# Performance work log

Hardware: AMD Instinct MI355X
Metric: run time of the kernel (lower is better)

The kernel has to match this reference:

```python
import jax, jax.numpy as jnp
import numpy as np

DIM = 768      # model dim
H = 12         # heads
HD = DIM // H  # head dim = 64
T = 8          # num_frames // 2 (video temporal frames)
SF = 8         # spec_frames (audio temporal frames)
AP = 196       # audio patches per frame
VP = 196       # video patches per frame
B = 4          # batch
SCALE = HD ** (-0.5)  # 0.125


def setup_inputs() -> dict:
    key = jax.random.key(0)
    ks = jax.random.split(key, 12)
    n = lambda k, shape, s=1.0: s * jax.random.normal(k, shape, dtype=jnp.float32)
    return {
        "s_x": n(ks[0], (2 + AP, B * SF, DIM)),
        "t_x": n(ks[1], (1 + VP, B * T, DIM)),
        "clip_space_pos": n(ks[2], (AP, DIM), SCALE),
        "vmae_space_pos": n(ks[3], (VP, DIM), SCALE),
        "clip_temporal_pos": n(ks[4], (SF, DIM), SCALE),
        "vmae_temporal_pos": n(ks[5], (T, DIM), SCALE),
        "q_w": n(ks[6], (DIM, DIM), 0.02),
        "q_b": jnp.zeros((DIM,), jnp.float32),
        "kv_w": n(ks[7], (2 * DIM, DIM), 0.02),
        "kv_b": jnp.zeros((2 * DIM,), jnp.float32),
        "proj_w": n(ks[8], (DIM, DIM), 0.02),
        "proj_b": jnp.zeros((DIM,), jnp.float32),
    }


def _prep(pat, space_pos, temp_pos, tt):
    # pat: (n, b*tt, d) ; rearrange 'n (b t) d -> b t n d', add space pos,
    # 'b t n d -> b n t d', add temporal pos, 'b n t d -> b (n t) d'
    n, bt, d = pat.shape
    b = bt // tt
    x = pat.reshape(n, b, tt, d).transpose(1, 2, 0, 3)      # b t n d
    x = x + space_pos                                        # (n,d) bcast
    x = x.transpose(0, 2, 1, 3) + temp_pos                   # b n t d + (t,d)
    return x.reshape(b, n * tt, d)


def reference(s_x, t_x, clip_space_pos, vmae_space_pos, clip_temporal_pos,
              vmae_temporal_pos, q_w, q_b, kv_w, kv_b, proj_w, proj_b):
    t_x_cls = t_x[:1]                                        # (1, b*T, d)
    s_pat = _prep(s_x[2:], clip_space_pos, clip_temporal_pos, SF)   # (b, AP*SF, d)
    t_pat = _prep(t_x[1:], vmae_space_pos, vmae_temporal_pos, T)    # (b, VP*T, d)

    b, N, d = t_pat.shape
    M = s_pat.shape[1]
    q = t_pat @ q_w.T + q_b                                  # (b, N, d)
    q = q.reshape(b, N, H, HD).transpose(0, 2, 1, 3)         # b h n hd
    kv = s_pat @ kv_w.T + kv_b                               # (b, M, 2d)
    kv = kv.reshape(b, M, 2, H, HD).transpose(2, 0, 3, 1, 4) # 2 b h m hd
    k, v = kv[0], kv[1]

    attn = jax.nn.softmax(jnp.einsum('bhnd,bhmd->bhnm', q * SCALE, k), axis=-1)
    out = jnp.einsum('bhnm,bhmd->bhnd', attn, v)             # b h n hd
    out = out.transpose(0, 2, 1, 3).reshape(b, N, d)         # b n d
    out = out @ proj_w.T + proj_b

    # 'b (n t) d -> n (b t) d'
    out = out.reshape(b, VP, T, d).transpose(1, 0, 2, 3).reshape(VP, b * T, d)
    return jnp.concatenate([t_x_cls, out], axis=0)           # (1+VP, b*T, d)
```

## Files before the change

### kernel.cpp

```cpp
#include <hip/hip_runtime.h>
#include <hip/hip_bf16.h>

#define DIM 768
#define NH 12
#define HD 64
#define NSEQ 1568
#define ROWS 6272
#define QSC2 0.18033688011112042f
#define AST 72

typedef __attribute__((ext_vector_type(8))) short short8;
typedef __attribute__((ext_vector_type(4))) float f32x4;
typedef __attribute__((ext_vector_type(4))) unsigned short u16x4;
typedef unsigned short ushort_t;
typedef unsigned int uint_t;

static __device__ __forceinline__ ushort_t f2bf(float f) {
    union { float f; uint_t u; } c; c.f = f;
    uint_t u = c.u + 0x7fffu + ((c.u >> 16) & 1u);
    return (ushort_t)(u >> 16);
}
static __device__ __forceinline__ int cvt_pk_bf16(float lo, float hi) {
    int r;
    asm("v_cvt_pk_bf16_f32 %0, %1, %2" : "=v"(r) : "v"(lo), "v"(hi));
    return r;
}
static __device__ __forceinline__ void glds16(const short* g, short* l) {
    __builtin_amdgcn_global_load_lds(
        (const __attribute__((address_space(1))) void*)g,
        (__attribute__((address_space(3))) void*)l, 16, 0, 0);
}

#define SM_HALF(S, PF, LR)                                                    \
    {                                                                         \
        float p_[4][4];                                                       \
        _Pragma("unroll")                                                     \
        for (int jb = 0; jb < 4; ++jb) {                                      \
            _Pragma("unroll")                                                 \
            for (int r = 0; r < 4; ++r)                                       \
                p_[jb][r] = __builtin_amdgcn_exp2f(S[jb][r]);                 \
        }                                                                     \
        float rs_ = ((p_[0][0] + p_[0][1]) + (p_[0][2] + p_[0][3]))           \
                  + ((p_[1][0] + p_[1][1]) + (p_[1][2] + p_[1][3]))           \
                  + ((p_[2][0] + p_[2][1]) + (p_[2][2] + p_[2][3]))           \
                  + ((p_[3][0] + p_[3][1]) + (p_[3][2] + p_[3][3]));          \
        rs_ += __shfl_xor(rs_, 16);                                           \
        rs_ += __shfl_xor(rs_, 32);                                           \
        LR += rs_;                                                            \
        int pw_[4][2];                                                        \
        _Pragma("unroll")                                                     \
        for (int jb = 0; jb < 4; ++jb) {                                      \
            pw_[jb][0] = cvt_pk_bf16(p_[jb][0], p_[jb][1]);                   \
            pw_[jb][1] = cvt_pk_bf16(p_[jb][2], p_[jb][3]);                   \
        }                                                                     \
        _Pragma("unroll")                                                     \
        for (int jb2 = 0; jb2 < 2; ++jb2) {                                   \
            int S0_ = gh ? pw_[jb2 * 2 + 1][0] : pw_[jb2 * 2][0];             \
            int S1_ = gh ? pw_[jb2 * 2 + 1][1] : pw_[jb2 * 2][1];             \
            union { int i[4]; short8 s; } fr_;                                \
            fr_.i[0] = __builtin_amdgcn_ds_bpermute(addr0, S0_);              \
            fr_.i[1] = __builtin_amdgcn_ds_bpermute(addr0, S1_);              \
            fr_.i[2] = __builtin_amdgcn_ds_bpermute(addr1, S0_);              \
            fr_.i[3] = __builtin_amdgcn_ds_bpermute(addr1, S1_);              \
            PF[jb2] = fr_.s;                                                  \
        }                                                                     \
    }

#define PREP_HALF (ROWS * (DIM / 8))
__global__ __launch_bounds__(256)
void prep2_bf(const float* __restrict__ src_t, const float* __restrict__ src_s,
              const float* __restrict__ vsp, const float* __restrict__ csp,
              const float* __restrict__ vtp, const float* __restrict__ ctp,
              short* __restrict__ dst_t, short* __restrict__ dst_s) {
    int idx = blockIdx.x * 256 + threadIdx.x;
    if (idx >= 2 * PREP_HALF) return;
    int sel = idx >= PREP_HALF;
    int i0  = sel ? idx - PREP_HALF : idx;
    const float* src  = sel ? src_s : src_t;
    const float* spos = sel ? csp : vsp;
    const float* tpos = sel ? ctp : vtp;
    short* dst = sel ? dst_s : dst_t;
    int d8  = i0 % (DIM / 8);
    int row = i0 / (DIM / 8);
    int b = row / NSEQ;
    int i = row % NSEQ;
    int n = i >> 3;
    int t = i & 7;
    const float4* s4 = reinterpret_cast<const float4*>(src + ((size_t)n * 32 + b * 8 + t) * DIM + d8 * 8);
    const float4* p4 = reinterpret_cast<const float4*>(spos + (size_t)n * DIM + d8 * 8);
    const float4* q4 = reinterpret_cast<const float4*>(tpos + (size_t)t * DIM + d8 * 8);
    union { int w[4]; short8 v; } o;
    float4 a0 = s4[0], a1 = s4[1], b0 = p4[0], b1 = p4[1], c0 = q4[0], c1 = q4[1];
    o.w[0] = cvt_pk_bf16(a0.x + b0.x + c0.x, a0.y + b0.y + c0.y);
    o.w[1] = cvt_pk_bf16(a0.z + b0.z + c0.z, a0.w + b0.w + c0.w);
    o.w[2] = cvt_pk_bf16(a1.x + b1.x + c1.x, a1.y + b1.y + c1.y);
    o.w[3] = cvt_pk_bf16(a1.z + b1.z + c1.z, a1.w + b1.w + c1.w);
    reinterpret_cast<short8*>(dst)[i0] = o.v;
}

#define W8 (DIM * DIM / 8)
__global__ __launch_bounds__(256)
void conv3_bf(const float* __restrict__ qw, const float* __restrict__ kvw,
              const float* __restrict__ pw, short* __restrict__ dq,
              short* __restrict__ dkv, short* __restrict__ dp) {
    int idx = blockIdx.x * 256 + threadIdx.x;
    if (idx >= 4 * W8) return;
    const float* src; short* dst; int off;
    if (idx < W8)            { src = qw;  dst = dq;  off = idx; }
    else if (idx < 3 * W8)   { src = kvw; dst = dkv; off = idx - W8; }
    else                     { src = pw;  dst = dp;  off = idx - 3 * W8; }
    const float4* s4 = reinterpret_cast<const float4*>(src + (size_t)off * 8);
    float4 a0 = s4[0], a1 = s4[1];
    union { int w[4]; short8 v; } o;
    o.w[0] = cvt_pk_bf16(a0.x, a0.y);
    o.w[1] = cvt_pk_bf16(a0.z, a0.w);
    o.w[2] = cvt_pk_bf16(a1.x, a1.y);
    o.w[3] = cvt_pk_bf16(a1.z, a1.w);
    reinterpret_cast<short8*>(dst)[off] = o.v;
}

__global__ __launch_bounds__(256)
void cls_kernel(const float* __restrict__ src, float* __restrict__ dst) {
    int idx = blockIdx.x * 256 + threadIdx.x;
    if (idx < 32 * DIM / 4)
        reinterpret_cast<float4*>(dst)[idx] = reinterpret_cast<const float4*>(src)[idx];
}

__global__ __launch_bounds__(256)
void gemm_qkv(const short* __restrict__ tpat, const short* __restrict__ spat,
              const short* __restrict__ wq, const short* __restrict__ wkv,
              const float* __restrict__ q_b, const float* __restrict__ kv_b,
              ushort_t* __restrict__ qout, ushort_t* __restrict__ kout,
              ushort_t* __restrict__ vtout) {
    __shared__ short As[128 * 32];
    __shared__ short Ws[128 * 32];
    const int t = threadIdx.x;
    const int l = t & 63, w = t >> 6;
    const int li = l & 15, g = l >> 4;
    const int mode = (blockIdx.x >= 6);
    const short* A  = mode ? spat : tpat;
    const short* Wm = mode ? wkv : wq;
    const float* bias = mode ? kv_b : q_b;
    const int c0 = (mode ? (int)blockIdx.x - 6 : (int)blockIdx.x) * 128;
    const int r0 = blockIdx.y * 128;
    const int wrow = (w >> 1) * 64, wcol = (w & 1) * 64;

    f32x4 acc[4][4];
    #pragma unroll
    for (int i = 0; i < 4; ++i)
        #pragma unroll
        for (int j = 0; j < 4; ++j) acc[i][j] = (f32x4){0.f, 0.f, 0.f, 0.f};

    const short* Ag = A  + (size_t)(r0 + w * 32 + (l >> 2)) * DIM + (l & 3) * 8;
    const short* Wg = Wm + (size_t)(c0 + w * 32 + (l >> 2)) * DIM + (l & 3) * 8;
    short* Al0 = &As[(w * 32) * 32];
    short* Al1 = &As[(w * 32 + 16) * 32];
    short* Wl0 = &Ws[(w * 32) * 32];
    short* Wl1 = &Ws[(w * 32 + 16) * 32];

    for (int k0 = 0; k0 < DIM; k0 += 32) {
        glds16(Ag + k0,                       Al0);
        glds16(Ag + (size_t)16 * DIM + k0,    Al1);
        glds16(Wg + k0,                       Wl0);
        glds16(Wg + (size_t)16 * DIM + k0,    Wl1);
        __syncthreads();
        short8 af[4], wf[4];
        #pragma unroll
        for (int mi = 0; mi < 4; ++mi)
            af[mi] = *reinterpret_cast<const short8*>(&As[(wrow + mi * 16 + li) * 32 + g * 8]);
        #pragma unroll
        for (int ni = 0; ni < 4; ++ni)
            wf[ni] = *reinterpret_cast<const short8*>(&Ws[(wcol + ni * 16 + li) * 32 + g * 8]);
        __builtin_amdgcn_s_setprio(1);
        #pragma unroll
        for (int mi = 0; mi < 4; ++mi)
            #pragma unroll
            for (int ni = 0; ni < 4; ++ni)
                acc[mi][ni] = __builtin_amdgcn_mfma_f32_16x16x32_bf16(af[mi], wf[ni], acc[mi][ni], 0, 0, 0);
        __builtin_amdgcn_s_setprio(0);
        __syncthreads();
    }

    #pragma unroll
    for (int mi = 0; mi < 4; ++mi) {
        int rowbase = r0 + wrow + mi * 16 + g * 4;
        int b = rowbase / NSEQ;
        int ii = rowbase - b * NSEQ;
        #pragma unroll
        for (int ni = 0; ni < 4; ++ni) {
            int c = c0 + wcol + ni * 16 + li;
            float bv = bias[c];
            if (mode == 0) {
                int h = c >> 6, e = c & 63;
                size_t base = (((size_t)b * NH + h) * NSEQ + ii) * HD + e;
                #pragma unroll
                for (int rr = 0; rr < 4; ++rr)
                    qout[base + (size_t)rr * HD] = f2bf((acc[mi][ni][rr] + bv) * QSC2);
            } else {
                if (c < DIM) {
                    int h = c >> 6, e = c & 63;
                    size_t base = (((size_t)b * NH + h) * NSEQ + ii) * HD + e;
                    #pragma unroll
                    for (int rr = 0; rr < 4; ++rr)
                        kout[base + (size_t)rr * HD] = f2bf(acc[mi][ni][rr] + bv);
                } else {
                    int cc = c - DIM;
                    int h = cc >> 6, e = cc & 63;
                    union { int w2[2]; u16x4 v; } pk;
                    pk.w2[0] = cvt_pk_bf16(acc[mi][ni][0] + bv, acc[mi][ni][1] + bv);
                    pk.w2[1] = cvt_pk_bf16(acc[mi][ni][2] + bv, acc[mi][ni][3] + bv);
                    *reinterpret_cast<u16x4*>(vtout + (((size_t)b * NH + h) * HD + e) * NSEQ + ii) = pk.v;
                }
            }
        }
    }
}

__global__ __launch_bounds__(256)
void gemm_proj(const short* __restrict__ A, const short* __restrict__ Wm,
               const float* __restrict__ bias, float* __restrict__ out) {
    __shared__ short As[128 * 32];
    __shared__ short Ws[128 * 32];
    const int t = threadIdx.x;
    const int l = t & 63, w = t >> 6;
    const int li = l & 15, g = l >> 4;
    const int c0 = blockIdx.x * 128, r0 = blockIdx.y * 128;
    const int wrow = (w >> 1) * 64, wcol = (w & 1) * 64;

    f32x4 acc[4][4];
    #pragma unroll
    for (int i = 0; i < 4; ++i)
        #pragma unroll
        for (int j = 0; j < 4; ++j) acc[i][j] = (f32x4){0.f, 0.f, 0.f, 0.f};

    const short* Ag = A  + (size_t)(r0 + w * 32 + (l >> 2)) * DIM + (l & 3) * 8;
    const short* Wg = Wm + (size_t)(c0 + w * 32 + (l >> 2)) * DIM + (l & 3) * 8;
    short* Al0 = &As[(w * 32) * 32];
    short* Al1 = &As[(w * 32 + 16) * 32];
    short* Wl0 = &Ws[(w * 32) * 32];
    short* Wl1 = &Ws[(w * 32 + 16) * 32];

    for (int k0 = 0; k0 < DIM; k0 += 32) {
        glds16(Ag + k0,                       Al0);
        glds16(Ag + (size_t)16 * DIM + k0,    Al1);
        glds16(Wg + k0,                       Wl0);
        glds16(Wg + (size_t)16 * DIM + k0,    Wl1);
        __syncthreads();
        short8 af[4], wf[4];
        #pragma unroll
        for (int mi = 0; mi < 4; ++mi)
            af[mi] = *reinterpret_cast<const short8*>(&As[(wrow + mi * 16 + li) * 32 + g * 8]);
        #pragma unroll
        for (int ni = 0; ni < 4; ++ni)
            wf[ni] = *reinterpret_cast<const short8*>(&Ws[(wcol + ni * 16 + li) * 32 + g * 8]);
        __builtin_amdgcn_s_setprio(1);
        #pragma unroll
        for (int mi = 0; mi < 4; ++mi)
            #pragma unroll
            for (int ni = 0; ni < 4; ++ni)
                acc[mi][ni] = __builtin_amdgcn_mfma_f32_16x16x32_bf16(af[mi], wf[ni], acc[mi][ni], 0, 0, 0);
        __builtin_amdgcn_s_setprio(0);
        __syncthreads();
    }

    #pragma unroll
    for (int mi = 0; mi < 4; ++mi) {
        int rowbase = r0 + wrow + mi * 16 + g * 4;
        int b = rowbase / NSEQ;
        int ii = rowbase - b * NSEQ;
        #pragma unroll
        for (int ni = 0; ni < 4; ++ni) {
            int c = c0 + wcol + ni * 16 + li;
            float bv = bias[c];
            #pragma unroll
            for (int rr = 0; rr < 4; ++rr) {
                int i2 = ii + rr;
                int n = i2 >> 3, tt = i2 & 7;
                out[((size_t)(1 + n) * 32 + b * 8 + tt) * DIM + c] = acc[mi][ni][rr] + bv;
            }
        }
    }
}

__global__ __launch_bounds__(256)
void attn_bf(const short* __restrict__ q, const short* __restrict__ k,
             const short* __restrict__ vt, ushort_t* __restrict__ ao) {
    __shared__ short Ks[2 * 64 * AST];
    __shared__ short Vs[2 * 64 * AST];
    const int t = threadIdx.x, l = t & 63, w = t >> 6;
    const int li = l & 15, g = l >> 4;
    const int bh = blockIdx.y, b = bh / NH, h = bh % NH;
    const int q0 = blockIdx.x * 128;
    const short* qb = q + (size_t)bh * NSEQ * HD;
    const short* kb = k + (size_t)bh * NSEQ * HD;
    const short* vb = vt + (size_t)bh * HD * NSEQ;
    const int row = t >> 2, ch = t & 3;

    short8 qf0[2], qf1[2];
    {
        int r_ = q0 + w * 32 + li;
        int rs = (r_ < NSEQ) ? r_ : 0;
        const short* s = qb + (size_t)rs * HD + g * 8;
        qf0[0] = *reinterpret_cast<const short8*>(s);
        qf0[1] = *reinterpret_cast<const short8*>(s + 32);
        r_ += 16;
        rs = (r_ < NSEQ) ? r_ : 0;
        s = qb + (size_t)rs * HD + g * 8;
        qf1[0] = *reinterpret_cast<const short8*>(s);
        qf1[1] = *reinterpret_cast<const short8*>(s + 32);
    }

    short8 kr0, kr1, vr0, vr1;
    {
        const short* s = kb + (size_t)row * HD + ch * 16;
        kr0 = *reinterpret_cast<const short8*>(s);
        kr1 = *reinterpret_cast<const short8*>(s + 8);
        const short* vs = vb + (size_t)row * NSEQ + ch * 16;
        vr0 = *reinterpret_cast<const short8*>(vs);
        vr1 = *reinterpret_cast<const short8*>(vs + 8);
    }
    *reinterpret_cast<short8*>(&Ks[row * AST + ch * 16])     = kr0;
    *reinterpret_cast<short8*>(&Ks[row * AST + ch * 16 + 8]) = kr1;
    *reinterpret_cast<short8*>(&Vs[row * AST + ch * 16])     = vr0;
    *reinterpret_cast<short8*>(&Vs[row * AST + ch * 16 + 8]) = vr1;

    f32x4 o0[4], o1[4];
    #pragma unroll
    for (int i = 0; i < 4; ++i) {
        o0[i] = (f32x4){0.f, 0.f, 0.f, 0.f};
        o1[i] = (f32x4){0.f, 0.f, 0.f, 0.f};
    }
    float lr0 = 0.f, lr1 = 0.f;
    const int addr0 = (li + ((2 * g) & 3) * 16) * 4;
    const int addr1 = (li + ((2 * g + 1) & 3) * 16) * 4;
    const int gh = g >> 1;

    int cur = 0;
    for (int m0 = 0; m0 < NSEQ; m0 += 64, cur ^= 1) {
        const short* Kc = &Ks[cur * 64 * AST];
        const short* Vc = &Vs[cur * 64 * AST];
        short* Kn = &Ks[(cur ^ 1) * 64 * AST];
        short* Vn = &Vs[(cur ^ 1) * 64 * AST];
        __syncthreads();
        const int m1 = m0 + 64;
        if (m1 < NSEQ) {
            int rs = (m1 + row < NSEQ) ? m1 + row : 0;
            const short* s = kb + (size_t)rs * HD + ch * 16;
            kr0 = *reinterpret_cast<const short8*>(s);
            kr1 = *reinterpret_cast<const short8*>(s + 8);
            int cs = (m1 + ch * 16 < NSEQ) ? ch : 0;
            const short* vs = vb + (size_t)row * NSEQ + m1 + cs * 16;
            vr0 = *reinterpret_cast<const short8*>(vs);
            vr1 = *reinterpret_cast<const short8*>(vs + 8);
        }

        f32x4 s0[4], s1[4];
        #pragma unroll
        for (int i = 0; i < 4; ++i) {
            s0[i] = (f32x4){0.f, 0.f, 0.f, 0.f};
            s1[i] = (f32x4){0.f, 0.f, 0.f, 0.f};
        }
        __builtin_amdgcn_s_setprio(1);
        #pragma unroll
        for (int jb = 0; jb < 4; ++jb) {
            short8 kf0 = *reinterpret_cast<const short8*>(&Kc[(jb * 16 + li) * AST + g * 8]);
            short8 kf1 = *reinterpret_cast<const short8*>(&Kc[(jb * 16 + li) * AST + 32 + g * 8]);
            s0[jb] = __builtin_amdgcn_mfma_f32_16x16x32_bf16(kf0, qf0[0], s0[jb], 0, 0, 0);
            s0[jb] = __builtin_amdgcn_mfma_f32_16x16x32_bf16(kf1, qf0[1], s0[jb], 0, 0, 0);
            s1[jb] = __builtin_amdgcn_mfma_f32_16x16x32_bf16(kf0, qf1[0], s1[jb], 0, 0, 0);
            s1[jb] = __builtin_amdgcn_mfma_f32_16x16x32_bf16(kf1, qf1[1], s1[jb], 0, 0, 0);
        }
        __builtin_amdgcn_s_setprio(0);
        if (m0 + 64 > NSEQ) {
            #pragma unroll
            for (int jb = 0; jb < 4; ++jb)
                #pragma unroll
                for (int r = 0; r < 4; ++r)
                    if (m0 + jb * 16 + g * 4 + r >= NSEQ) {
                        s0[jb][r] = -1e30f;
                        s1[jb][r] = -1e30f;
                    }
        }

        short8 pf0[2], pf1[2];
        SM_HALF(s0, pf0, lr0)
        SM_HALF(s1, pf1, lr1)

        if (m1 < NSEQ) {
            *reinterpret_cast<short8*>(&Kn[row * AST + ch * 16])     = kr0;
            *reinterpret_cast<short8*>(&Kn[row * AST + ch * 16 + 8]) = kr1;
            *reinterpret_cast<short8*>(&Vn[row * AST + ch * 16])     = vr0;
            *reinterpret_cast<short8*>(&Vn[row * AST + ch * 16 + 8]) = vr1;
        }

        __builtin_amdgcn_s_setprio(1);
        #pragma unroll
        for (int nb = 0; nb < 4; ++nb)
            #pragma unroll
            for (int jb2 = 0; jb2 < 2; ++jb2) {
                short8 vf = *reinterpret_cast<const short8*>(&Vc[(nb * 16 + li) * AST + jb2 * 32 + g * 8]);
                o0[nb] = __builtin_amdgcn_mfma_f32_16x16x32_bf16(vf, pf0[jb2], o0[nb], 0, 0, 0);
                o1[nb] = __builtin_amdgcn_mfma_f32_16x16x32_bf16(vf, pf1[jb2], o1[nb], 0, 0, 0);
            }
        __builtin_amdgcn_s_setprio(0);
    }

    {
        int orow = q0 + w * 32 + li;
        if (orow < NSEQ) {
            float invl = 1.f / lr0;
            ushort_t* ob = ao + ((size_t)b * NSEQ + orow) * DIM + h * HD;
            #pragma unroll
            for (int nb = 0; nb < 4; ++nb) {
                union { int w2[2]; u16x4 v; } pk;
                pk.w2[0] = cvt_pk_bf16(o0[nb][0] * invl, o0[nb][1] * invl);
                pk.w2[1] = cvt_pk_bf16(o0[nb][2] * invl, o0[nb][3] * invl);
                *reinterpret_cast<u16x4*>(ob + nb * 16 + g * 4) = pk.v;
            }
        }
    }
    {
        int orow = q0 + w * 32 + 16 + li;
        if (orow < NSEQ) {
            float invl = 1.f / lr1;
            ushort_t* ob = ao + ((size_t)b * NSEQ + orow) * DIM + h * HD;
            #pragma unroll
            for (int nb = 0; nb < 4; ++nb) {
                union { int w2[2]; u16x4 v; } pk;
                pk.w2[0] = cvt_pk_bf16(o1[nb][0] * invl, o1[nb][1] * invl);
                pk.w2[1] = cvt_pk_bf16(o1[nb][2] * invl, o1[nb][3] * invl);
                *reinterpret_cast<u16x4*>(ob + nb * 16 + g * 4) = pk.v;
            }
        }
    }
}

extern "C" void kernel_launch(void* const* d_in, const int* in_sizes, int n_in,
                              void* d_out, int out_size, void* d_ws, size_t ws_size,
                              hipStream_t stream) {
    const float* s_x    = (const float*)d_in[0];
    const float* t_x    = (const float*)d_in[1];
    const float* csp    = (const float*)d_in[2];
    const float* vsp    = (const float*)d_in[3];
    const float* ctp    = (const float*)d_in[4];
    const float* vtp    = (const float*)d_in[5];
    const float* q_w    = (const float*)d_in[6];
    const float* q_b    = (const float*)d_in[7];
    const float* kv_w   = (const float*)d_in[8];
    const float* kv_b   = (const float*)d_in[9];
    const float* proj_w = (const float*)d_in[10];
    const float* proj_b = (const float*)d_in[11];
    float* out = (float*)d_out;

    const size_t S2 = (size_t)ROWS * DIM;
    short* tpat = (short*)d_ws;
    short* spat = tpat + S2;
    short* qbf  = spat + S2;
    short* kbf  = qbf + S2;
    short* vtbf = kbf + S2;
    short* wq   = vtbf + S2;
    short* wkv  = wq + (size_t)DIM * DIM;
    short* wp   = wkv + (size_t)2 * DIM * DIM;

    prep2_bf<<<(2 * PREP_HALF + 255) / 256, 256, 0, stream>>>(
        t_x + (size_t)32 * DIM, s_x + (size_t)64 * DIM, vsp, csp, vtp, ctp, tpat, spat);
    conv3_bf<<<(4 * W8 + 255) / 256, 256, 0, stream>>>(q_w, kv_w, proj_w, wq, wkv, wp);
    cls_kernel<<<24, 256, 0, stream>>>(t_x, out);

    gemm_qkv<<<dim3(18, 49), 256, 0, stream>>>(tpat, spat, wq, wkv, q_b, kv_b,
                                               (ushort_t*)qbf, (ushort_t*)kbf, (ushort_t*)vtbf);
    attn_bf<<<dim3(13, 48), 256, 0, stream>>>(qbf, kbf, vtbf, (ushort_t*)tpat);
    gemm_proj<<<dim3(6, 49), 256, 0, stream>>>(tpat, wp, proj_b, out);
}
```

Measured before the change: 152.0 us.

## Split attention KV range in two and merge partial outputs in a new kernel

The attention kernel now splits the key/value sequence into two ranges via a third grid dimension. Each half writes unnormalized fp32 partial outputs and row sums to workspace. A new merge kernel adds the two halves, normalizes and writes bf16 output. This doubles the number of blocks to improve CU occupancy and wave balance, at the cost of extra fp32 global traffic and one more kernel launch.

```diff
diff --git a/kernel.cpp b/kernel.cpp
--- a/kernel.cpp
+++ b/kernel.cpp
@@ -8,6 +8,7 @@
 #define ROWS 6272
 #define QSC2 0.18033688011112042f
 #define AST 72
+#define SPLIT_M 832
 
 typedef __attribute__((ext_vector_type(8))) short short8;
 typedef __attribute__((ext_vector_type(4))) float f32x4;
@@ -284,12 +285,16 @@
 
 __global__ __launch_bounds__(256)
 void attn_bf(const short* __restrict__ q, const short* __restrict__ k,
-             const short* __restrict__ vt, ushort_t* __restrict__ ao) {
+             const short* __restrict__ vt, float* __restrict__ opart,
+             float* __restrict__ lpart) {
     __shared__ short Ks[2 * 64 * AST];
     __shared__ short Vs[2 * 64 * AST];
     const int t = threadIdx.x, l = t & 63, w = t >> 6;
     const int li = l & 15, g = l >> 4;
-    const int bh = blockIdx.y, b = bh / NH, h = bh % NH;
+    const int bh = blockIdx.y;
+    const int sp = blockIdx.z;
+    const int m_start = sp ? SPLIT_M : 0;
+    const int m_end   = sp ? NSEQ : SPLIT_M;
     const int q0 = blockIdx.x * 128;
     const short* qb = q + (size_t)bh * NSEQ * HD;
     const short* kb = k + (size_t)bh * NSEQ * HD;
@@ -312,10 +317,10 @@
 
     short8 kr0, kr1, vr0, vr1;
     {
-        const short* s = kb + (size_t)row * HD + ch * 16;
+        const short* s = kb + (size_t)(m_start + row) * HD + ch * 16;
         kr0 = *reinterpret_cast<const short8*>(s);
         kr1 = *reinterpret_cast<const short8*>(s + 8);
-        const short* vs = vb + (size_t)row * NSEQ + ch * 16;
+        const short* vs = vb + (size_t)row * NSEQ + m_start + ch * 16;
         vr0 = *reinterpret_cast<const short8*>(vs);
         vr1 = *reinterpret_cast<const short8*>(vs + 8);
     }
@@ -336,14 +341,14 @@
     const int gh = g >> 1;
 
     int cur = 0;
-    for (int m0 = 0; m0 < NSEQ; m0 += 64, cur ^= 1) {
+    for (int m0 = m_start; m0 < m_end; m0 += 64, cur ^= 1) {
         const short* Kc = &Ks[cur * 64 * AST];
         const short* Vc = &Vs[cur * 64 * AST];
         short* Kn = &Ks[(cur ^ 1) * 64 * AST];
         short* Vn = &Vs[(cur ^ 1) * 64 * AST];
         __syncthreads();
         const int m1 = m0 + 64;
-        if (m1 < NSEQ) {
+        if (m1 < m_end) {
             int rs = (m1 + row < NSEQ) ? m1 + row : 0;
             const short* s = kb + (size_t)rs * HD + ch * 16;
             kr0 = *reinterpret_cast<const short8*>(s);
@@ -386,7 +391,7 @@
         SM_HALF(s0, pf0, lr0)
         SM_HALF(s1, pf1, lr1)
 
-        if (m1 < NSEQ) {
+        if (m1 < m_end) {
             *reinterpret_cast<short8*>(&Kn[row * AST + ch * 16])     = kr0;
             *reinterpret_cast<short8*>(&Kn[row * AST + ch * 16 + 8]) = kr1;
             *reinterpret_cast<short8*>(&Vn[row * AST + ch * 16])     = vr0;
@@ -408,31 +413,48 @@
     {
         int orow = q0 + w * 32 + li;
         if (orow < NSEQ) {
-            float invl = 1.f / lr0;
-            ushort_t* ob = ao + ((size_t)b * NSEQ + orow) * DIM + h * HD;
-            #pragma unroll
-            for (int nb = 0; nb < 4; ++nb) {
-                union { int w2[2]; u16x4 v; } pk;
-                pk.w2[0] = cvt_pk_bf16(o0[nb][0] * invl, o0[nb][1] * invl);
-                pk.w2[1] = cvt_pk_bf16(o0[nb][2] * invl, o0[nb][3] * invl);
-                *reinterpret_cast<u16x4*>(ob + nb * 16 + g * 4) = pk.v;
-            }
+            float* op = opart + (((size_t)sp * 48 + bh) * NSEQ + orow) * HD + g * 4;
+            #pragma unroll
+            for (int nb = 0; nb < 4; ++nb)
+                *reinterpret_cast<f32x4*>(op + nb * 16) = o0[nb];
         }
     }
     {
         int orow = q0 + w * 32 + 16 + li;
         if (orow < NSEQ) {
-            float invl = 1.f / lr1;
-            ushort_t* ob = ao + ((size_t)b * NSEQ + orow) * DIM + h * HD;
-            #pragma unroll
-            for (int nb = 0; nb < 4; ++nb) {
-                union { int w2[2]; u16x4 v; } pk;
-                pk.w2[0] = cvt_pk_bf16(o1[nb][0] * invl, o1[nb][1] * invl);
-                pk.w2[1] = cvt_pk_bf16(o1[nb][2] * invl, o1[nb][3] * invl);
-                *reinterpret_cast<u16x4*>(ob + nb * 16 + g * 4) = pk.v;
-            }
-        }
-    }
+            float* op = opart + (((size_t)sp * 48 + bh) * NSEQ + orow) * HD + g * 4;
+            #pragma unroll
+            for (int nb = 0; nb < 4; ++nb)
+                *reinterpret_cast<f32x4*>(op + nb * 16) = o1[nb];
+        }
+    }
+    if (l < 16) {
+        int r_ = q0 + w * 32 + l;
+        float* lp = lpart + ((size_t)sp * 48 + bh) * NSEQ;
+        if (r_ < NSEQ)      lp[r_]      = lr0;
+        if (r_ + 16 < NSEQ) lp[r_ + 16] = lr1;
+    }
+}
+
+__global__ __launch_bounds__(256)
+void merge_bf(const float* __restrict__ opart, const float* __restrict__ lpart,
+              ushort_t* __restrict__ ao) {
+    const int bh = blockIdx.y;
+    int tid = blockIdx.x * 256 + threadIdx.x;
+    int row = tid >> 4, e4 = (tid & 15) * 4;
+    const size_t base = ((size_t)bh * NSEQ + row) * HD + e4;
+    const size_t so = (size_t)48 * NSEQ * HD;
+    f32x4 a = *reinterpret_cast<const f32x4*>(opart + base);
+    f32x4 c = *reinterpret_cast<const f32x4*>(opart + so + base);
+    float l0 = lpart[(size_t)bh * NSEQ + row];
+    float l1 = lpart[(size_t)48 * NSEQ + (size_t)bh * NSEQ + row];
+    float inv = 1.f / (l0 + l1);
+    int b = bh / NH, h = bh - b * NH;
+    ushort_t* ob = ao + ((size_t)b * NSEQ + row) * DIM + h * HD + e4;
+    union { int w2[2]; u16x4 v; } pk;
+    pk.w2[0] = cvt_pk_bf16((a[0] + c[0]) * inv, (a[1] + c[1]) * inv);
+    pk.w2[1] = cvt_pk_bf16((a[2] + c[2]) * inv, (a[3] + c[3]) * inv);
+    *reinterpret_cast<u16x4*>(ob) = pk.v;
 }
 
 extern "C" void kernel_launch(void* const* d_in, const int* in_sizes, int n_in,
@@ -461,6 +483,8 @@
     short* wq   = vtbf + S2;
     short* wkv  = wq + (size_t)DIM * DIM;
     short* wp   = wkv + (size_t)2 * DIM * DIM;
+    float* opart = (float*)(wp + (size_t)DIM * DIM);
+    float* lpart = opart + (size_t)2 * 48 * NSEQ * HD;
 
     prep2_bf<<<(2 * PREP_HALF + 255) / 256, 256, 0, stream>>>(
         t_x + (size_t)32 * DIM, s_x + (size_t)64 * DIM, vsp, csp, vtp, ctp, tpat, spat);
@@ -469,6 +493,7 @@
 
     gemm_qkv<<<dim3(18, 49), 256, 0, stream>>>(tpat, spat, wq, wkv, q_b, kv_b,
                                                (ushort_t*)qbf, (ushort_t*)kbf, (ushort_t*)vtbf);
-    attn_bf<<<dim3(13, 48), 256, 0, stream>>>(qbf, kbf, vtbf, (ushort_t*)tpat);
+    attn_bf<<<dim3(13, 48, 2), 256, 0, stream>>>(qbf, kbf, vtbf, opart, lpart);
+    merge_bf<<<dim3(98, 48), 256, 0, stream>>>(opart, lpart, (ushort_t*)tpat);
     gemm_proj<<<dim3(6, 49), 256, 0, stream>>>(tpat, wp, proj_b, out);
 }
```

After: 167.1 us. 1.1x slower.

## Load attention K/V fragments directly from global, remap grid, fuse prep kernels

Applied to the files above, without the earlier changes.

The attention kernel drops its double-buffered LDS staging and syncthreads and instead loads K and V^T MFMA fragments straight from global memory into registers, prefetching the next K tile during softmax. Bounds clamping is removed and the workspace gets padding so overreads stay in bounds. The grid is flattened and remapped so that groups of eight heads share the same query tile, which should improve L2 reuse. The three prep kernels are merged into one launch. The trade-off is more global/L2 traffic per wave and higher register pressure, since K/V are no longer shared across the four waves of a block.

```diff
diff --git a/kernel.cpp b/kernel.cpp
--- a/kernel.cpp
+++ b/kernel.cpp
@@ -7,7 +7,6 @@
 #define NSEQ 1568
 #define ROWS 6272
 #define QSC2 0.18033688011112042f
-#define AST 72
 
 typedef __attribute__((ext_vector_type(8))) short short8;
 typedef __attribute__((ext_vector_type(4))) float f32x4;
@@ -67,63 +66,59 @@
     }
 
 #define PREP_HALF (ROWS * (DIM / 8))
+#define W8 (DIM * DIM / 8)
+#define CLS4 (32 * DIM / 4)
 __global__ __launch_bounds__(256)
-void prep2_bf(const float* __restrict__ src_t, const float* __restrict__ src_s,
+void prep_all(const float* __restrict__ src_t, const float* __restrict__ src_s,
               const float* __restrict__ vsp, const float* __restrict__ csp,
               const float* __restrict__ vtp, const float* __restrict__ ctp,
-              short* __restrict__ dst_t, short* __restrict__ dst_s) {
+              const float* __restrict__ qw, const float* __restrict__ kvw,
+              const float* __restrict__ pw, const float* __restrict__ txc,
+              short* __restrict__ dst_t, short* __restrict__ dst_s,
+              short* __restrict__ dq, short* __restrict__ dkv,
+              short* __restrict__ dp, float* __restrict__ out_cls) {
     int idx = blockIdx.x * 256 + threadIdx.x;
-    if (idx >= 2 * PREP_HALF) return;
-    int sel = idx >= PREP_HALF;
-    int i0  = sel ? idx - PREP_HALF : idx;
-    const float* src  = sel ? src_s : src_t;
-    const float* spos = sel ? csp : vsp;
-    const float* tpos = sel ? ctp : vtp;
-    short* dst = sel ? dst_s : dst_t;
-    int d8  = i0 % (DIM / 8);
-    int row = i0 / (DIM / 8);
-    int b = row / NSEQ;
-    int i = row % NSEQ;
-    int n = i >> 3;
-    int t = i & 7;
-    const float4* s4 = reinterpret_cast<const float4*>(src + ((size_t)n * 32 + b * 8 + t) * DIM + d8 * 8);
-    const float4* p4 = reinterpret_cast<const float4*>(spos + (size_t)n * DIM + d8 * 8);
-    const float4* q4 = reinterpret_cast<const float4*>(tpos + (size_t)t * DIM + d8 * 8);
-    union { int w[4]; short8 v; } o;
-    float4 a0 = s4[0], a1 = s4[1], b0 = p4[0], b1 = p4[1], c0 = q4[0], c1 = q4[1];
-    o.w[0] = cvt_pk_bf16(a0.x + b0.x + c0.x, a0.y + b0.y + c0.y);
-    o.w[1] = cvt_pk_bf16(a0.z + b0.z + c0.z, a0.w + b0.w + c0.w);
-    o.w[2] = cvt_pk_bf16(a1.x + b1.x + c1.x, a1.y + b1.y + c1.y);
-    o.w[3] = cvt_pk_bf16(a1.z + b1.z + c1.z, a1.w + b1.w + c1.w);
-    reinterpret_cast<short8*>(dst)[i0] = o.v;
-}
-
-#define W8 (DIM * DIM / 8)
-__global__ __launch_bounds__(256)
-void conv3_bf(const float* __restrict__ qw, const float* __restrict__ kvw,
-              const float* __restrict__ pw, short* __restrict__ dq,
-              short* __restrict__ dkv, short* __restrict__ dp) {
-    int idx = blockIdx.x * 256 + threadIdx.x;
-    if (idx >= 4 * W8) return;
-    const float* src; short* dst; int off;
-    if (idx < W8)            { src = qw;  dst = dq;  off = idx; }
-    else if (idx < 3 * W8)   { src = kvw; dst = dkv; off = idx - W8; }
-    else                     { src = pw;  dst = dp;  off = idx - 3 * W8; }
-    const float4* s4 = reinterpret_cast<const float4*>(src + (size_t)off * 8);
-    float4 a0 = s4[0], a1 = s4[1];
-    union { int w[4]; short8 v; } o;
-    o.w[0] = cvt_pk_bf16(a0.x, a0.y);
-    o.w[1] = cvt_pk_bf16(a0.z, a0.w);
-    o.w[2] = cvt_pk_bf16(a1.x, a1.y);
-    o.w[3] = cvt_pk_bf16(a1.z, a1.w);
-    reinterpret_cast<short8*>(dst)[off] = o.v;
-}
-
-__global__ __launch_bounds__(256)
-void cls_kernel(const float* __restrict__ src, float* __restrict__ dst) {
-    int idx = blockIdx.x * 256 + threadIdx.x;
-    if (idx < 32 * DIM / 4)
-        reinterpret_cast<float4*>(dst)[idx] = reinterpret_cast<const float4*>(src)[idx];
+    if (idx < 2 * PREP_HALF) {
+        int sel = idx >= PREP_HALF;
+        int i0  = sel ? idx - PREP_HALF : idx;
+        const float* src  = sel ? src_s : src_t;
+        const float* spos = sel ? csp : vsp;
+        const float* tpos = sel ? ctp : vtp;
+        short* dst = sel ? dst_s : dst_t;
+        int d8  = i0 % (DIM / 8);
+        int row = i0 / (DIM / 8);
+        int b = row / NSEQ;
+        int i = row % NSEQ;
+        int n = i >> 3;
+        int t = i & 7;
+        const float4* s4 = reinterpret_cast<const float4*>(src + ((size_t)n * 32 + b * 8 + t) * DIM + d8 * 8);
+        const float4* p4 = reinterpret_cast<const float4*>(spos + (size_t)n * DIM + d8 * 8);
+        const float4* q4 = reinterpret_cast<const float4*>(tpos + (size_t)t * DIM + d8 * 8);
+        union { int w[4]; short8 v; } o;
+        float4 a0 = s4[0], a1 = s4[1], b0 = p4[0], b1 = p4[1], c0 = q4[0], c1 = q4[1];
+        o.w[0] = cvt_pk_bf16(a0.x + b0.x + c0.x, a0.y + b0.y + c0.y);
+        o.w[1] = cvt_pk_bf16(a0.z + b0.z + c0.z, a0.w + b0.w + c0.w);
+        o.w[2] = cvt_pk_bf16(a1.x + b1.x + c1.x, a1.y + b1.y + c1.y);
+        o.w[3] = cvt_pk_bf16(a1.z + b1.z + c1.z, a1.w + b1.w + c1.w);
+        reinterpret_cast<short8*>(dst)[i0] = o.v;
+    } else if (idx < 2 * PREP_HALF + 4 * W8) {
+        int i0 = idx - 2 * PREP_HALF;
+        const float* src; short* dst; int off;
+        if (i0 < W8)            { src = qw;  dst = dq;  off = i0; }
+        else if (i0 < 3 * W8)   { src = kvw; dst = dkv; off = i0 - W8; }
+        else                    { src = pw;  dst = dp;  off = i0 - 3 * W8; }
+        const float4* s4 = reinterpret_cast<const float4*>(src + (size_t)off * 8);
+        float4 a0 = s4[0], a1 = s4[1];
+        union { int w[4]; short8 v; } o;
+        o.w[0] = cvt_pk_bf16(a0.x, a0.y);
+        o.w[1] = cvt_pk_bf16(a0.z, a0.w);
+        o.w[2] = cvt_pk_bf16(a1.x, a1.y);
+        o.w[3] = cvt_pk_bf16(a1.z, a1.w);
+        reinterpret_cast<short8*>(dst)[off] = o.v;
+    } else {
+        int i0 = idx - (2 * PREP_HALF + 4 * W8);
+        reinterpret_cast<float4*>(out_cls)[i0] = reinterpret_cast<const float4*>(txc)[i0];
+    }
 }
 
 __global__ __launch_bounds__(256)
@@ -285,44 +280,27 @@
 __global__ __launch_bounds__(256)
 void attn_bf(const short* __restrict__ q, const short* __restrict__ k,
              const short* __restrict__ vt, ushort_t* __restrict__ ao) {
-    __shared__ short Ks[2 * 64 * AST];
-    __shared__ short Vs[2 * 64 * AST];
     const int t = threadIdx.x, l = t & 63, w = t >> 6;
     const int li = l & 15, g = l >> 4;
-    const int bh = blockIdx.y, b = bh / NH, h = bh % NH;
-    const int q0 = blockIdx.x * 128;
+    const int bid = blockIdx.x;
+    const int rest = bid >> 3;
+    const int bh = (bid & 7) + 8 * (rest / 13);
+    const int qx = rest % 13;
+    const int b = bh / NH, h = bh % NH;
+    const int q0 = qx * 128;
     const short* qb = q + (size_t)bh * NSEQ * HD;
-    const short* kb = k + (size_t)bh * NSEQ * HD;
-    const short* vb = vt + (size_t)bh * HD * NSEQ;
-    const int row = t >> 2, ch = t & 3;
+    const short* kl = k + (size_t)bh * NSEQ * HD + (size_t)li * HD + g * 8;
+    const short* vl = vt + (size_t)bh * HD * NSEQ + (size_t)li * NSEQ + g * 8;
 
     short8 qf0[2], qf1[2];
     {
-        int r_ = q0 + w * 32 + li;
-        int rs = (r_ < NSEQ) ? r_ : 0;
-        const short* s = qb + (size_t)rs * HD + g * 8;
+        const short* s = qb + (size_t)(q0 + w * 32 + li) * HD + g * 8;
         qf0[0] = *reinterpret_cast<const short8*>(s);
         qf0[1] = *reinterpret_cast<const short8*>(s + 32);
-        r_ += 16;
-        rs = (r_ < NSEQ) ? r_ : 0;
-        s = qb + (size_t)rs * HD + g * 8;
+        s += 16 * HD;
         qf1[0] = *reinterpret_cast<const short8*>(s);
         qf1[1] = *reinterpret_cast<const short8*>(s + 32);
     }
-
-    short8 kr0, kr1, vr0, vr1;
-    {
-        const short* s = kb + (size_t)row * HD + ch * 16;
-        kr0 = *reinterpret_cast<const short8*>(s);
-        kr1 = *reinterpret_cast<const short8*>(s + 8);
-        const short* vs = vb + (size_t)row * NSEQ + ch * 16;
-        vr0 = *reinterpret_cast<const short8*>(vs);
-        vr1 = *reinterpret_cast<const short8*>(vs + 8);
-    }
-    *reinterpret_cast<short8*>(&Ks[row * AST + ch * 16])     = kr0;
-    *reinterpret_cast<short8*>(&Ks[row * AST + ch * 16 + 8]) = kr1;
-    *reinterpret_cast<short8*>(&Vs[row * AST + ch * 16])     = vr0;
-    *reinterpret_cast<short8*>(&Vs[row * AST + ch * 16 + 8]) = vr1;
 
     f32x4 o0[4], o1[4];
     #pragma unroll
@@ -335,23 +313,21 @@
     const int addr1 = (li + ((2 * g + 1) & 3) * 16) * 4;
     const int gh = g >> 1;
 
-    int cur = 0;
-    for (int m0 = 0; m0 < NSEQ; m0 += 64, cur ^= 1) {
-        const short* Kc = &Ks[cur * 64 * AST];
-        const short* Vc = &Vs[cur * 64 * AST];
-        short* Kn = &Ks[(cur ^ 1) * 64 * AST];
-        short* Vn = &Vs[(cur ^ 1) * 64 * AST];
-        __syncthreads();
-        const int m1 = m0 + 64;
-        if (m1 < NSEQ) {
-            int rs = (m1 + row < NSEQ) ? m1 + row : 0;
-            const short* s = kb + (size_t)rs * HD + ch * 16;
-            kr0 = *reinterpret_cast<const short8*>(s);
-            kr1 = *reinterpret_cast<const short8*>(s + 8);
-            int cs = (m1 + ch * 16 < NSEQ) ? ch : 0;
-            const short* vs = vb + (size_t)row * NSEQ + m1 + cs * 16;
-            vr0 = *reinterpret_cast<const short8*>(vs);
-            vr1 = *reinterpret_cast<const short8*>(vs + 8);
+    short8 kf[4][2];
+    #pragma unroll
+    for (int jb = 0; jb < 4; ++jb) {
+        const short* s = kl + (size_t)(jb * 16) * HD;
+        kf[jb][0] = *reinterpret_cast<const short8*>(s);
+        kf[jb][1] = *reinterpret_cast<const short8*>(s + 32);
+    }
+
+    for (int m0 = 0; m0 < NSEQ; m0 += 64) {
+        short8 vf[4][2];
+        #pragma unroll
+        for (int nb = 0; nb < 4; ++nb) {
+            const short* s = vl + (size_t)(nb * 16) * NSEQ + m0;
+            vf[nb][0] = *reinterpret_cast<const short8*>(s);
+            vf[nb][1] = *reinterpret_cast<const short8*>(s + 32);
         }
 
         f32x4 s0[4], s1[4];
@@ -363,14 +339,22 @@
         __builtin_amdgcn_s_setprio(1);
         #pragma unroll
         for (int jb = 0; jb < 4; ++jb) {
-            short8 kf0 = *reinterpret_cast<const short8*>(&Kc[(jb * 16 + li) * AST + g * 8]);
-            short8 kf1 = *reinterpret_cast<const short8*>(&Kc[(jb * 16 + li) * AST + 32 + g * 8]);
-            s0[jb] = __builtin_amdgcn_mfma_f32_16x16x32_bf16(kf0, qf0[0], s0[jb], 0, 0, 0);
-            s0[jb] = __builtin_amdgcn_mfma_f32_16x16x32_bf16(kf1, qf0[1], s0[jb], 0, 0, 0);
-            s1[jb] = __builtin_amdgcn_mfma_f32_16x16x32_bf16(kf0, qf1[0], s1[jb], 0, 0, 0);
-            s1[jb] = __builtin_amdgcn_mfma_f32_16x16x32_bf16(kf1, qf1[1], s1[jb], 0, 0, 0);
+            s0[jb] = __builtin_amdgcn_mfma_f32_16x16x32_bf16(kf[jb][0], qf0[0], s0[jb], 0, 0, 0);
+            s0[jb] = __builtin_amdgcn_mfma_f32_16x16x32_bf16(kf[jb][1], qf0[1], s0[jb], 0, 0, 0);
+            s1[jb] = __builtin_amdgcn_mfma_f32_16x16x32_bf16(kf[jb][0], qf1[0], s1[jb], 0, 0, 0);
+            s1[jb] = __builtin_amdgcn_mfma_f32_16x16x32_bf16(kf[jb][1], qf1[1], s1[jb], 0, 0, 0);
         }
         __builtin_amdgcn_s_setprio(0);
+
+        if (m0 + 64 < NSEQ) {
+            #pragma unroll
+            for (int jb = 0; jb < 4; ++jb) {
+                const short* s = kl + (size_t)(m0 + 64 + jb * 16) * HD;
+                kf[jb][0] = *reinterpret_cast<const short8*>(s);
+                kf[jb][1] = *reinterpret_cast<const short8*>(s + 32);
+            }
+        }
+
         if (m0 + 64 > NSEQ) {
             #pragma unroll
             for (int jb = 0; jb < 4; ++jb)
@@ -386,21 +370,13 @@
         SM_HALF(s0, pf0, lr0)
         SM_HALF(s1, pf1, lr1)
 
-        if (m1 < NSEQ) {
-            *reinterpret_cast<short8*>(&Kn[row * AST + ch * 16])     = kr0;
-            *reinterpret_cast<short8*>(&Kn[row * AST + ch * 16 + 8]) = kr1;
-            *reinterpret_cast<short8*>(&Vn[row * AST + ch * 16])     = vr0;
-            *reinterpret_cast<short8*>(&Vn[row * AST + ch * 16 + 8]) = vr1;
-        }
-
         __builtin_amdgcn_s_setprio(1);
         #pragma unroll
         for (int nb = 0; nb < 4; ++nb)
             #pragma unroll
             for (int jb2 = 0; jb2 < 2; ++jb2) {
-                short8 vf = *reinterpret_cast<const short8*>(&Vc[(nb * 16 + li) * AST + jb2 * 32 + g * 8]);
-                o0[nb] = __builtin_amdgcn_mfma_f32_16x16x32_bf16(vf, pf0[jb2], o0[nb], 0, 0, 0);
-                o1[nb] = __builtin_amdgcn_mfma_f32_16x16x32_bf16(vf, pf1[jb2], o1[nb], 0, 0, 0);
+                o0[nb] = __builtin_amdgcn_mfma_f32_16x16x32_bf16(vf[nb][jb2], pf0[jb2], o0[nb], 0, 0, 0);
+                o1[nb] = __builtin_amdgcn_mfma_f32_16x16x32_bf16(vf[nb][jb2], pf1[jb2], o1[nb], 0, 0, 0);
             }
         __builtin_amdgcn_s_setprio(0);
     }
@@ -453,22 +429,22 @@
     float* out = (float*)d_out;
 
     const size_t S2 = (size_t)ROWS * DIM;
+    const size_t SLACK = 8192;
     short* tpat = (short*)d_ws;
     short* spat = tpat + S2;
     short* qbf  = spat + S2;
-    short* kbf  = qbf + S2;
-    short* vtbf = kbf + S2;
-    short* wq   = vtbf + S2;
+    short* kbf  = qbf + S2 + SLACK;
+    short* vtbf = kbf + S2 + SLACK;
+    short* wq   = vtbf + S2 + SLACK;
     short* wkv  = wq + (size_t)DIM * DIM;
     short* wp   = wkv + (size_t)2 * DIM * DIM;
 
-    prep2_bf<<<(2 * PREP_HALF + 255) / 256, 256, 0, stream>>>(
-        t_x + (size_t)32 * DIM, s_x + (size_t)64 * DIM, vsp, csp, vtp, ctp, tpat, spat);
-    conv3_bf<<<(4 * W8 + 255) / 256, 256, 0, stream>>>(q_w, kv_w, proj_w, wq, wkv, wp);
-    cls_kernel<<<24, 256, 0, stream>>>(t_x, out);
+    prep_all<<<5880, 256, 0, stream>>>(
+        t_x + (size_t)32 * DIM, s_x + (size_t)64 * DIM, vsp, csp, vtp, ctp,
+        q_w, kv_w, proj_w, t_x, tpat, spat, wq, wkv, wp, out);
 
     gemm_qkv<<<dim3(18, 49), 256, 0, stream>>>(tpat, spat, wq, wkv, q_b, kv_b,
                                                (ushort_t*)qbf, (ushort_t*)kbf, (ushort_t*)vtbf);
-    attn_bf<<<dim3(13, 48), 256, 0, stream>>>(qbf, kbf, vtbf, (ushort_t*)tpat);
+    attn_bf<<<624, 256, 0, stream>>>(qbf, kbf, vtbf, (ushort_t*)tpat);
     gemm_proj<<<dim3(6, 49), 256, 0, stream>>>(tpat, wp, proj_b, out);
 }
```

Result: slower. 189.8 us (+24.9%).

## Double-buffer GEMM LDS tiles, remap blocks across XCDs, merge prep launches

Applied to the files above, without the earlier changes.

Both bf16 GEMM kernels now use two LDS buffers, so the global-to-LDS load for the next K-tile is issued before the MFMAs on the current tile. This is meant to hide memory latency behind compute, and it doubles shared memory per block. The GEMM grids are flattened to 1D and remapped so that consecutive tiles land on the same XCD, which should improve L2 reuse of shared A and W panels. The three small preprocessing kernels (activation prep, weight conversion, CLS copy) are merged into one launch to cut launch overhead.

```diff
diff --git a/kernel.cpp b/kernel.cpp
--- a/kernel.cpp
+++ b/kernel.cpp
@@ -67,63 +67,59 @@
     }
 
 #define PREP_HALF (ROWS * (DIM / 8))
+#define W8 (DIM * DIM / 8)
+#define CLS4 (32 * DIM / 4)
 __global__ __launch_bounds__(256)
-void prep2_bf(const float* __restrict__ src_t, const float* __restrict__ src_s,
+void prep_all(const float* __restrict__ src_t, const float* __restrict__ src_s,
               const float* __restrict__ vsp, const float* __restrict__ csp,
               const float* __restrict__ vtp, const float* __restrict__ ctp,
-              short* __restrict__ dst_t, short* __restrict__ dst_s) {
+              const float* __restrict__ qw, const float* __restrict__ kvw,
+              const float* __restrict__ pw, const float* __restrict__ txc,
+              short* __restrict__ dst_t, short* __restrict__ dst_s,
+              short* __restrict__ dq, short* __restrict__ dkv,
+              short* __restrict__ dp, float* __restrict__ out_cls) {
     int idx = blockIdx.x * 256 + threadIdx.x;
-    if (idx >= 2 * PREP_HALF) return;
-    int sel = idx >= PREP_HALF;
-    int i0  = sel ? idx - PREP_HALF : idx;
-    const float* src  = sel ? src_s : src_t;
-    const float* spos = sel ? csp : vsp;
-    const float* tpos = sel ? ctp : vtp;
-    short* dst = sel ? dst_s : dst_t;
-    int d8  = i0 % (DIM / 8);
-    int row = i0 / (DIM / 8);
-    int b = row / NSEQ;
-    int i = row % NSEQ;
-    int n = i >> 3;
-    int t = i & 7;
-    const float4* s4 = reinterpret_cast<const float4*>(src + ((size_t)n * 32 + b * 8 + t) * DIM + d8 * 8);
-    const float4* p4 = reinterpret_cast<const float4*>(spos + (size_t)n * DIM + d8 * 8);
-    const float4* q4 = reinterpret_cast<const float4*>(tpos + (size_t)t * DIM + d8 * 8);
-    union { int w[4]; short8 v; } o;
-    float4 a0 = s4[0], a1 = s4[1], b0 = p4[0], b1 = p4[1], c0 = q4[0], c1 = q4[1];
-    o.w[0] = cvt_pk_bf16(a0.x + b0.x + c0.x, a0.y + b0.y + c0.y);
-    o.w[1] = cvt_pk_bf16(a0.z + b0.z + c0.z, a0.w + b0.w + c0.w);
-    o.w[2] = cvt_pk_bf16(a1.x + b1.x + c1.x, a1.y + b1.y + c1.y);
-    o.w[3] = cvt_pk_bf16(a1.z + b1.z + c1.z, a1.w + b1.w + c1.w);
-    reinterpret_cast<short8*>(dst)[i0] = o.v;
-}
-
-#define W8 (DIM * DIM / 8)
-__global__ __launch_bounds__(256)
-void conv3_bf(const float* __restrict__ qw, const float* __restrict__ kvw,
-              const float* __restrict__ pw, short* __restrict__ dq,
-              short* __restrict__ dkv, short* __restrict__ dp) {
-    int idx = blockIdx.x * 256 + threadIdx.x;
-    if (idx >= 4 * W8) return;
-    const float* src; short* dst; int off;
-    if (idx < W8)            { src = qw;  dst = dq;  off = idx; }
-    else if (idx < 3 * W8)   { src = kvw; dst = dkv; off = idx - W8; }
-    else                     { src = pw;  dst = dp;  off = idx - 3 * W8; }
-    const float4* s4 = reinterpret_cast<const float4*>(src + (size_t)off * 8);
-    float4 a0 = s4[0], a1 = s4[1];
-    union { int w[4]; short8 v; } o;
-    o.w[0] = cvt_pk_bf16(a0.x, a0.y);
-    o.w[1] = cvt_pk_bf16(a0.z, a0.w);
-    o.w[2] = cvt_pk_bf16(a1.x, a1.y);
-    o.w[3] = cvt_pk_bf16(a1.z, a1.w);
-    reinterpret_cast<short8*>(dst)[off] = o.v;
-}
-
-__global__ __launch_bounds__(256)
-void cls_kernel(const float* __restrict__ src, float* __restrict__ dst) {
-    int idx = blockIdx.x * 256 + threadIdx.x;
-    if (idx < 32 * DIM / 4)
-        reinterpret_cast<float4*>(dst)[idx] = reinterpret_cast<const float4*>(src)[idx];
+    if (idx < 2 * PREP_HALF) {
+        int sel = idx >= PREP_HALF;
+        int i0  = sel ? idx - PREP_HALF : idx;
+        const float* src  = sel ? src_s : src_t;
+        const float* spos = sel ? csp : vsp;
+        const float* tpos = sel ? ctp : vtp;
+        short* dst = sel ? dst_s : dst_t;
+        int d8  = i0 % (DIM / 8);
+        int row = i0 / (DIM / 8);
+        int b = row / NSEQ;
+        int i = row % NSEQ;
+        int n = i >> 3;
+        int t = i & 7;
+        const float4* s4 = reinterpret_cast<const float4*>(src + ((size_t)n * 32 + b * 8 + t) * DIM + d8 * 8);
+        const float4* p4 = reinterpret_cast<const float4*>(spos + (size_t)n * DIM + d8 * 8);
+        const float4* q4 = reinterpret_cast<const float4*>(tpos + (size_t)t * DIM + d8 * 8);
+        union { int w[4]; short8 v; } o;
+        float4 a0 = s4[0], a1 = s4[1], b0 = p4[0], b1 = p4[1], c0 = q4[0], c1 = q4[1];
+        o.w[0] = cvt_pk_bf16(a0.x + b0.x + c0.x, a0.y + b0.y + c0.y);
+        o.w[1] = cvt_pk_bf16(a0.z + b0.z + c0.z, a0.w + b0.w + c0.w);
+        o.w[2] = cvt_pk_bf16(a1.x + b1.x + c1.x, a1.y + b1.y + c1.y);
+        o.w[3] = cvt_pk_bf16(a1.z + b1.z + c1.z, a1.w + b1.w + c1.w);
+        reinterpret_cast<short8*>(dst)[i0] = o.v;
+    } else if (idx < 2 * PREP_HALF + 4 * W8) {
+        int i0 = idx - 2 * PREP_HALF;
+        const float* src; short* dst; int off;
+        if (i0 < W8)            { src = qw;  dst = dq;  off = i0; }
+        else if (i0 < 3 * W8)   { src = kvw; dst = dkv; off = i0 - W8; }
+        else                    { src = pw;  dst = dp;  off = i0 - 3 * W8; }
+        const float4* s4 = reinterpret_cast<const float4*>(src + (size_t)off * 8);
+        float4 a0 = s4[0], a1 = s4[1];
+        union { int w[4]; short8 v; } o;
+        o.w[0] = cvt_pk_bf16(a0.x, a0.y);
+        o.w[1] = cvt_pk_bf16(a0.z, a0.w);
+        o.w[2] = cvt_pk_bf16(a1.x, a1.y);
+        o.w[3] = cvt_pk_bf16(a1.z, a1.w);
+        reinterpret_cast<short8*>(dst)[off] = o.v;
+    } else {
+        int i0 = idx - (2 * PREP_HALF + 4 * W8);
+        reinterpret_cast<float4*>(out_cls)[i0] = reinterpret_cast<const float4*>(txc)[i0];
+    }
 }
 
 __global__ __launch_bounds__(256)
@@ -132,17 +128,21 @@
               const float* __restrict__ q_b, const float* __restrict__ kv_b,
               ushort_t* __restrict__ qout, ushort_t* __restrict__ kout,
               ushort_t* __restrict__ vtout) {
-    __shared__ short As[128 * 32];
-    __shared__ short Ws[128 * 32];
+    __shared__ short As[2][128 * 32];
+    __shared__ short Ws[2][128 * 32];
     const int t = threadIdx.x;
     const int l = t & 63, w = t >> 6;
     const int li = l & 15, g = l >> 4;
-    const int mode = (blockIdx.x >= 6);
+    int orig = blockIdx.x;
+    int xcd = orig & 7, idxq = orig >> 3;
+    int wg = (xcd < 2 ? xcd * 111 : 222 + (xcd - 2) * 110) + idxq;
+    const int x = wg % 18, y = wg / 18;
+    const int mode = (x >= 6);
     const short* A  = mode ? spat : tpat;
     const short* Wm = mode ? wkv : wq;
     const float* bias = mode ? kv_b : q_b;
-    const int c0 = (mode ? (int)blockIdx.x - 6 : (int)blockIdx.x) * 128;
-    const int r0 = blockIdx.y * 128;
+    const int c0 = (mode ? x - 6 : x) * 128;
+    const int r0 = y * 128;
     const int wrow = (w >> 1) * 64, wcol = (w & 1) * 64;
 
     f32x4 acc[4][4];
@@ -153,24 +153,29 @@
 
     const short* Ag = A  + (size_t)(r0 + w * 32 + (l >> 2)) * DIM + (l & 3) * 8;
     const short* Wg = Wm + (size_t)(c0 + w * 32 + (l >> 2)) * DIM + (l & 3) * 8;
-    short* Al0 = &As[(w * 32) * 32];
-    short* Al1 = &As[(w * 32 + 16) * 32];
-    short* Wl0 = &Ws[(w * 32) * 32];
-    short* Wl1 = &Ws[(w * 32 + 16) * 32];
-
+
+    glds16(Ag,                    &As[0][(w * 32) * 32]);
+    glds16(Ag + (size_t)16 * DIM, &As[0][(w * 32 + 16) * 32]);
+    glds16(Wg,                    &Ws[0][(w * 32) * 32]);
+    glds16(Wg + (size_t)16 * DIM, &Ws[0][(w * 32 + 16) * 32]);
+    __syncthreads();
+
+    int cur = 0;
     for (int k0 = 0; k0 < DIM; k0 += 32) {
-        glds16(Ag + k0,                       Al0);
-        glds16(Ag + (size_t)16 * DIM + k0,    Al1);
-        glds16(Wg + k0,                       Wl0);
-        glds16(Wg + (size_t)16 * DIM + k0,    Wl1);
-        __syncthreads();
+        if (k0 + 32 < DIM) {
+            int nb = cur ^ 1;
+            glds16(Ag + k0 + 32,                    &As[nb][(w * 32) * 32]);
+            glds16(Ag + (size_t)16 * DIM + k0 + 32, &As[nb][(w * 32 + 16) * 32]);
+            glds16(Wg + k0 + 32,                    &Ws[nb][(w * 32) * 32]);
+            glds16(Wg + (size_t)16 * DIM + k0 + 32, &Ws[nb][(w * 32 + 16) * 32]);
+        }
         short8 af[4], wf[4];
         #pragma unroll
         for (int mi = 0; mi < 4; ++mi)
-            af[mi] = *reinterpret_cast<const short8*>(&As[(wrow + mi * 16 + li) * 32 + g * 8]);
+            af[mi] = *reinterpret_cast<const short8*>(&As[cur][(wrow + mi * 16 + li) * 32 + g * 8]);
         #pragma unroll
         for (int ni = 0; ni < 4; ++ni)
-            wf[ni] = *reinterpret_cast<const short8*>(&Ws[(wcol + ni * 16 + li) * 32 + g * 8]);
+            wf[ni] = *reinterpret_cast<const short8*>(&Ws[cur][(wcol + ni * 16 + li) * 32 + g * 8]);
         __builtin_amdgcn_s_setprio(1);
         #pragma unroll
         for (int mi = 0; mi < 4; ++mi)
@@ -179,6 +184,7 @@
                 acc[mi][ni] = __builtin_amdgcn_mfma_f32_16x16x32_bf16(af[mi], wf[ni], acc[mi][ni], 0, 0, 0);
         __builtin_amdgcn_s_setprio(0);
         __syncthreads();
+        cur ^= 1;
     }
 
     #pragma unroll
@@ -219,12 +225,15 @@
 __global__ __launch_bounds__(256)
 void gemm_proj(const short* __restrict__ A, const short* __restrict__ Wm,
                const float* __restrict__ bias, float* __restrict__ out) {
-    __shared__ short As[128 * 32];
-    __shared__ short Ws[128 * 32];
+    __shared__ short As[2][128 * 32];
+    __shared__ short Ws[2][128 * 32];
     const int t = threadIdx.x;
     const int l = t & 63, w = t >> 6;
     const int li = l & 15, g = l >> 4;
-    const int c0 = blockIdx.x * 128, r0 = blockIdx.y * 128;
+    int orig = blockIdx.x;
+    int xcd = orig & 7, idxq = orig >> 3;
+    int wg = (xcd < 6 ? xcd * 37 : 222 + (xcd - 6) * 36) + idxq;
+    const int c0 = (wg % 6) * 128, r0 = (wg / 6) * 128;
     const int wrow = (w >> 1) * 64, wcol = (w & 1) * 64;
 
     f32x4 acc[4][4];
@@ -235,24 +244,29 @@
 
     const short* Ag = A  + (size_t)(r0 + w * 32 + (l >> 2)) * DIM + (l & 3) * 8;
     const short* Wg = Wm + (size_t)(c0 + w * 32 + (l >> 2)) * DIM + (l & 3) * 8;
-    short* Al0 = &As[(w * 32) * 32];
-    short* Al1 = &As[(w * 32 + 16) * 32];
-    short* Wl0 = &Ws[(w * 32) * 32];
-    short* Wl1 = &Ws[(w * 32 + 16) * 32];
-
+
+    glds16(Ag,                    &As[0][(w * 32) * 32]);
+    glds16(Ag + (size_t)16 * DIM, &As[0][(w * 32 + 16) * 32]);
+    glds16(Wg,                    &Ws[0][(w * 32) * 32]);
+    glds16(Wg + (size_t)16 * DIM, &Ws[0][(w * 32 + 16) * 32]);
+    __syncthreads();
+
+    int cur = 0;
     for (int k0 = 0; k0 < DIM; k0 += 32) {
-        glds16(Ag + k0,                       Al0);
-        glds16(Ag + (size_t)16 * DIM + k0,    Al1);
-        glds16(Wg + k0,                       Wl0);
-        glds16(Wg + (size_t)16 * DIM + k0,    Wl1);
-        __syncthreads();
+        if (k0 + 32 < DIM) {
+            int nb = cur ^ 1;
+            glds16(Ag + k0 + 32,                    &As[nb][(w * 32) * 32]);
+            glds16(Ag + (size_t)16 * DIM + k0 + 32, &As[nb][(w * 32 + 16) * 32]);
+            glds16(Wg + k0 + 32,                    &Ws[nb][(w * 32) * 32]);
+            glds16(Wg + (size_t)16 * DIM + k0 + 32, &Ws[nb][(w * 32 + 16) * 32]);
+        }
         short8 af[4], wf[4];
         #pragma unroll
         for (int mi = 0; mi < 4; ++mi)
-            af[mi] = *reinterpret_cast<const short8*>(&As[(wrow + mi * 16 + li) * 32 + g * 8]);
+            af[mi] = *reinterpret_cast<const short8*>(&As[cur][(wrow + mi * 16 + li) * 32 + g * 8]);
         #pragma unroll
         for (int ni = 0; ni < 4; ++ni)
-            wf[ni] = *reinterpret_cast<const short8*>(&Ws[(wcol + ni * 16 + li) * 32 + g * 8]);
+            wf[ni] = *reinterpret_cast<const short8*>(&Ws[cur][(wcol + ni * 16 + li) * 32 + g * 8]);
         __builtin_amdgcn_s_setprio(1);
         #pragma unroll
         for (int mi = 0; mi < 4; ++mi)
@@ -261,6 +275,7 @@
                 acc[mi][ni] = __builtin_amdgcn_mfma_f32_16x16x32_bf16(af[mi], wf[ni], acc[mi][ni], 0, 0, 0);
         __builtin_amdgcn_s_setprio(0);
         __syncthreads();
+        cur ^= 1;
     }
 
     #pragma unroll
@@ -462,13 +477,12 @@
     short* wkv  = wq + (size_t)DIM * DIM;
     short* wp   = wkv + (size_t)2 * DIM * DIM;
 
-    prep2_bf<<<(2 * PREP_HALF + 255) / 256, 256, 0, stream>>>(
-        t_x + (size_t)32 * DIM, s_x + (size_t)64 * DIM, vsp, csp, vtp, ctp, tpat, spat);
-    conv3_bf<<<(4 * W8 + 255) / 256, 256, 0, stream>>>(q_w, kv_w, proj_w, wq, wkv, wp);
-    cls_kernel<<<24, 256, 0, stream>>>(t_x, out);
-
-    gemm_qkv<<<dim3(18, 49), 256, 0, stream>>>(tpat, spat, wq, wkv, q_b, kv_b,
-                                               (ushort_t*)qbf, (ushort_t*)kbf, (ushort_t*)vtbf);
+    prep_all<<<5880, 256, 0, stream>>>(
+        t_x + (size_t)32 * DIM, s_x + (size_t)64 * DIM, vsp, csp, vtp, ctp,
+        q_w, kv_w, proj_w, t_x, tpat, spat, wq, wkv, wp, out);
+
+    gemm_qkv<<<882, 256, 0, stream>>>(tpat, spat, wq, wkv, q_b, kv_b,
+                                      (ushort_t*)qbf, (ushort_t*)kbf, (ushort_t*)vtbf);
     attn_bf<<<dim3(13, 48), 256, 0, stream>>>(qbf, kbf, vtbf, (ushort_t*)tpat);
-    gemm_proj<<<dim3(6, 49), 256, 0, stream>>>(tpat, wp, proj_b, out);
-}
+    gemm_proj<<<294, 256, 0, stream>>>(tpat, wp, proj_b, out);
+}
```

Result: faster. 143.4 us (-5.6%).
